# Performance work log

Measured on AMD Instinct MI355X. Metric: run time of the kernel, lower is better.

## Reference

```python
import jax, jax.numpy as jnp
import numpy as np

PLOGIT_INIT = 1.5

def setup_inputs() -> dict:
    key = jax.random.key(0)
    B, C, H, W = 32, 256, 64, 64
    x = jax.random.normal(key, (B, C, H, W), dtype=jnp.float32)
    plogit = jnp.full((C,), PLOGIT_INIT, dtype=jnp.float32)  # learned param (post channel-expansion)
    return {"input": x, "plogit": plogit}


def reference(input, plogit):
    B, C = input.shape[0], input.shape[1]
    x = input.reshape(B * C, -1)                       # [B*C, HW]  (to_cw)
    s = jnp.sort(x, axis=-1)                           # per-row full sort
    N = s.shape[1]
    p = jax.nn.sigmoid(plogit)                         # [C]
    # torch: p.view(1,-1).repeat(B,1).view(-1) -> channel-major tiling over batch
    p_full = jnp.tile(p, B)                            # [B*C]
    # torch indexes with int(N * p.data[0] -/+ 0.02): a single scalar column index
    p0 = jax.lax.stop_gradient(p[0])
    i_low = jnp.clip((N * (p0 - 0.02)).astype(jnp.int32), 0, N - 1)
    i_high = jnp.clip((N * (p0 + 0.02)).astype(jnp.int32), 0, N - 1)
    x_low = jax.lax.stop_gradient(jnp.take(s, i_low, axis=1))    # [B*C], detached
    x_high = jax.lax.stop_gradient(jnp.take(s, i_high, axis=1))  # [B*C], detached
    thr = x_low + (x_high - x_low) * p_full            # linear interp, grad flows via p
    thr = thr.reshape(B, C, 1, 1)                      # from_cw
    return jax.nn.relu(input - thr)
```

## Files before the change

kernel.cpp:

```cpp
#include <hip/hip_runtime.h>
#include <math.h>

#define NTHREADS 256
#define WPB      4
#define NELEM    4096
#define EPL      64
#define NREP1    4
#define HSTRIDE  260
#define WAVE_LDS (NREP1 * HSTRIDE)
#define LDSW     (WPB * WAVE_LDS)

typedef float v4f __attribute__((ext_vector_type(4)));

__device__ __forceinline__ unsigned f2ord(float f) {
    unsigned u = __float_as_uint(f);
    return u ^ ((unsigned)((int)u >> 31) | 0x80000000u);
}
__device__ __forceinline__ float ord2f(unsigned k) {
    return __uint_as_float(k ^ (~(unsigned)((int)k >> 31) | 0x80000000u));
}

__device__ __forceinline__ unsigned iscan_dpp(unsigned v) {
    v += (unsigned)__builtin_amdgcn_update_dpp(0, (int)v, 0x111, 0xF, 0xF, false);
    v += (unsigned)__builtin_amdgcn_update_dpp(0, (int)v, 0x112, 0xF, 0xF, false);
    v += (unsigned)__builtin_amdgcn_update_dpp(0, (int)v, 0x114, 0xF, 0xF, false);
    v += (unsigned)__builtin_amdgcn_update_dpp(0, (int)v, 0x118, 0xF, 0xF, false);
    v += (unsigned)__builtin_amdgcn_update_dpp(0, (int)v, 0x142, 0xA, 0xF, false);
    v += (unsigned)__builtin_amdgcn_update_dpp(0, (int)v, 0x143, 0xC, 0xF, false);
    return v;
}

struct Pick2 { unsigned a, b; };

template <int NR>
__device__ __forceinline__ Pick2 wave_pick2(const unsigned* region, int lane,
                                            unsigned rA, unsigned rB) {
    unsigned s0 = 0, s1 = 0, s2 = 0, s3 = 0;
    #pragma unroll
    for (int rep = 0; rep < NR; ++rep) {
        uint4 h = ((const uint4*)(region + rep * HSTRIDE))[lane];
        s0 += h.x; s1 += h.y; s2 += h.z; s3 += h.w;
    }
    unsigned tot = s0 + s1 + s2 + s3;
    unsigned inc = iscan_dpp(tot);
    unsigned ex  = inc - tot;
    unsigned base[4] = {ex, ex + s0, ex + s0 + s1, ex + s0 + s1 + s2};
    unsigned cnt[4]  = {s0, s1, s2, s3};
    unsigned resA = 0, resB = 0;
    bool fA = false, fB = false;
    #pragma unroll
    for (int j = 0; j < 4; ++j) {
        if (rA >= base[j] && rA < base[j] + cnt[j]) {
            resA = ((unsigned)(4 * lane + j) << 12) | (rA - base[j]); fA = true;
        }
        if (rB >= base[j] && rB < base[j] + cnt[j]) {
            resB = ((unsigned)(4 * lane + j) << 12) | (rB - base[j]); fB = true;
        }
    }
    unsigned long long mA = __ballot(fA);
    unsigned long long mB = __ballot(fB);
    Pick2 r;
    r.a = (unsigned)__builtin_amdgcn_readlane((int)resA, (int)(__ffsll((long long)mA) - 1));
    r.b = (unsigned)__builtin_amdgcn_readlane((int)resB, (int)(__ffsll((long long)mB) - 1));
    return r;
}

__global__ void __launch_bounds__(NTHREADS, 4)
xsrelu_kernel(const float* __restrict__ x, const float* __restrict__ plogit,
              float* __restrict__ out, int C, int nrows) {
    __shared__ __align__(16) unsigned hist[LDSW];

    const int tid  = threadIdx.x;
    const int wid  = tid >> 6;
    const int lane = tid & 63;
    const int row  = blockIdx.x * WPB + wid;
    if (row >= nrows) return;

    unsigned* wbase = hist + wid * WAVE_LDS;

    const float4* xr = (const float4*)(x + (size_t)row * NELEM);
    unsigned k[EPL];
    #pragma unroll
    for (int j = 0; j < EPL / 4; ++j) {
        float4 v = xr[j * 64 + lane];
        k[4 * j + 0] = f2ord(v.x);
        k[4 * j + 1] = f2ord(v.y);
        k[4 * j + 2] = f2ord(v.z);
        k[4 * j + 3] = f2ord(v.w);
    }

    float p0 = 1.0f / (1.0f + expf(-plogit[0]));
    float pc = 1.0f / (1.0f + expf(-plogit[row % C]));
    int kLow  = min(max((int)((float)NELEM * (p0 - 0.02f)), 0), NELEM - 1);
    int kHigh = min(max((int)((float)NELEM * (p0 + 0.02f)), 0), NELEM - 1);

    unsigned* my1 = wbase + (lane & (NREP1 - 1)) * HSTRIDE;
    const uint4 z4 = make_uint4(0u, 0u, 0u, 0u);
    #pragma unroll
    for (int r = 0; r < NREP1; ++r)
        ((uint4*)(wbase + r * HSTRIDE))[lane] = z4;
    #pragma unroll
    for (int j = 0; j < EPL; ++j)
        atomicAdd(&my1[k[j] >> 24], 1u);
    Pick2 p1 = wave_pick2<NREP1>(wbase, lane, (unsigned)kLow, (unsigned)kHigh);
    unsigned bA = p1.a >> 12, bB = p1.b >> 12;
    unsigned prefA = bA << 24, rA = p1.a & 0xFFFu;
    unsigned prefB = bB << 24, rB = p1.b & 0xFFFu;
    unsigned known = 0xFF000000u;
    bool diverged = (bA != bB);

    unsigned* myT = wbase;
    unsigned* myB = wbase + HSTRIDE;
    #pragma unroll 1
    for (int shift = 16; shift >= 0; shift -= 8) {
        if (!diverged) {
            ((uint4*)myT)[lane] = z4;
            #pragma unroll
            for (int j = 0; j < EPL; ++j) {
                unsigned kk = k[j];
                if ((kk & known) == prefA)
                    atomicAdd(&myT[(kk >> shift) & 0xFFu], 1u);
            }
            Pick2 p = wave_pick2<1>(myT, lane, rA, rB);
            unsigned cA = p.a >> 12, cB = p.b >> 12;
            prefA |= cA << shift;  rA = p.a & 0xFFFu;
            prefB |= cB << shift;  rB = p.b & 0xFFFu;
            diverged = (cA != cB);
        } else {
            ((uint4*)myT)[lane] = z4;
            ((uint4*)myB)[lane] = z4;
            #pragma unroll
            for (int j = 0; j < EPL; ++j) {
                unsigned kk = k[j];
                unsigned km = kk & known;
                bool isB = (km == prefB);
                if ((km == prefA) | isB)
                    atomicAdd((isB ? myB : myT) + ((kk >> shift) & 0xFFu), 1u);
            }
            unsigned pa = wave_pick2<1>(myT, lane, rA, rA).a;
            unsigned pb = wave_pick2<1>(myB, lane, rB, rB).a;
            prefA |= (pa >> 12) << shift;  rA = pa & 0xFFFu;
            prefB |= (pb >> 12) << shift;  rB = pb & 0xFFFu;
        }
        known |= 0xFFu << shift;
    }

    float xlow  = ord2f(prefA);
    float xhigh = ord2f(prefB);
    float thr = xlow + (xhigh - xlow) * pc;

    v4f* outr = (v4f*)(out + (size_t)row * NELEM);
    #pragma unroll
    for (int j = 0; j < EPL / 4; ++j) {
        v4f o;
        o.x = fmaxf(ord2f(k[4 * j + 0]) - thr, 0.0f);
        o.y = fmaxf(ord2f(k[4 * j + 1]) - thr, 0.0f);
        o.z = fmaxf(ord2f(k[4 * j + 2]) - thr, 0.0f);
        o.w = fmaxf(ord2f(k[4 * j + 3]) - thr, 0.0f);
        __builtin_nontemporal_store(o, outr + j * 64 + lane);
    }
}

extern "C" void kernel_launch(void* const* d_in, const int* in_sizes, int n_in,
                              void* d_out, int out_size, void* d_ws, size_t ws_size,
                              hipStream_t stream) {
    const float* x      = (const float*)d_in[0];
    const float* plogit = (const float*)d_in[1];
    float* out          = (float*)d_out;
    int C    = in_sizes[1];
    int rows = in_sizes[0] / NELEM;
    int grid = (rows + WPB - 1) / WPB;
    xsrelu_kernel<<<grid, NTHREADS, 0, stream>>>(x, plogit, out, C, rows);
}
```

Measured before the change: 237.6 us.

## Split into block-per-row threshold kernel and separate streaming ReLU kernel

Replaces the single fused kernel, in which each wave handled one row with 64 keys held in registers, by two kernels. The first assigns one 256-thread block per row, stores the ordered keys in LDS and builds block-shared radix histograms with __syncthreads between passes, then writes a per-row threshold to workspace. The second is a grid-stride elementwise kernel that rereads x and applies relu(x - thr). The aim is to cut register pressure and raise parallelism in the selection phase, at the cost of reading x from memory a second time, adding a kernel launch, and adding block-wide barriers.

```diff
diff --git a/kernel.cpp b/kernel.cpp
--- a/kernel.cpp
+++ b/kernel.cpp
@@ -1,14 +1,14 @@
 #include <hip/hip_runtime.h>
 #include <math.h>
 
-#define NTHREADS 256
-#define WPB      4
 #define NELEM    4096
-#define EPL      64
-#define NREP1    4
+#define A_THREADS 256
 #define HSTRIDE  260
-#define WAVE_LDS (NREP1 * HSTRIDE)
-#define LDSW     (WPB * WAVE_LDS)
+#define NHREP    8
+#define A_LDSW   (NELEM + NHREP * HSTRIDE)
+
+#define B_THREADS 256
+#define B_BLOCKS  2048
 
 typedef float v4f __attribute__((ext_vector_type(4)));
 
@@ -65,99 +65,110 @@
     return r;
 }
 
-__global__ void __launch_bounds__(NTHREADS, 4)
-xsrelu_kernel(const float* __restrict__ x, const float* __restrict__ plogit,
-              float* __restrict__ out, int C, int nrows) {
-    __shared__ __align__(16) unsigned hist[LDSW];
+__global__ void __launch_bounds__(A_THREADS, 4)
+thr_kernel(const float* __restrict__ x, const float* __restrict__ plogit,
+           float* __restrict__ thr_out, int C) {
+    __shared__ __align__(16) unsigned keys[NELEM];
+    __shared__ __align__(16) unsigned hist[NHREP * HSTRIDE];
 
     const int tid  = threadIdx.x;
     const int wid  = tid >> 6;
     const int lane = tid & 63;
-    const int row  = blockIdx.x * WPB + wid;
-    if (row >= nrows) return;
-
-    unsigned* wbase = hist + wid * WAVE_LDS;
+    const int row  = blockIdx.x;
 
     const float4* xr = (const float4*)(x + (size_t)row * NELEM);
-    unsigned k[EPL];
+    unsigned* myrep = hist + wid * HSTRIDE;
+    const uint4 z4 = make_uint4(0u, 0u, 0u, 0u);
+
+    ((uint4*)myrep)[lane] = z4;
     #pragma unroll
-    for (int j = 0; j < EPL / 4; ++j) {
-        float4 v = xr[j * 64 + lane];
-        k[4 * j + 0] = f2ord(v.x);
-        k[4 * j + 1] = f2ord(v.y);
-        k[4 * j + 2] = f2ord(v.z);
-        k[4 * j + 3] = f2ord(v.w);
+    for (int j = 0; j < 4; ++j) {
+        int idx = wid * 256 + j * 64 + lane;
+        float4 v = xr[idx];
+        unsigned k0 = f2ord(v.x), k1 = f2ord(v.y), k2 = f2ord(v.z), k3 = f2ord(v.w);
+        ((uint4*)keys)[idx] = make_uint4(k0, k1, k2, k3);
+        atomicAdd(&myrep[k0 >> 24], 1u);
+        atomicAdd(&myrep[k1 >> 24], 1u);
+        atomicAdd(&myrep[k2 >> 24], 1u);
+        atomicAdd(&myrep[k3 >> 24], 1u);
     }
 
     float p0 = 1.0f / (1.0f + expf(-plogit[0]));
     float pc = 1.0f / (1.0f + expf(-plogit[row % C]));
-    int kLow  = min(max((int)((float)NELEM * (p0 - 0.02f)), 0), NELEM - 1);
-    int kHigh = min(max((int)((float)NELEM * (p0 + 0.02f)), 0), NELEM - 1);
+    unsigned kLow  = (unsigned)min(max((int)((float)NELEM * (p0 - 0.02f)), 0), NELEM - 1);
+    unsigned kHigh = (unsigned)min(max((int)((float)NELEM * (p0 + 0.02f)), 0), NELEM - 1);
 
-    unsigned* my1 = wbase + (lane & (NREP1 - 1)) * HSTRIDE;
-    const uint4 z4 = make_uint4(0u, 0u, 0u, 0u);
-    #pragma unroll
-    for (int r = 0; r < NREP1; ++r)
-        ((uint4*)(wbase + r * HSTRIDE))[lane] = z4;
-    #pragma unroll
-    for (int j = 0; j < EPL; ++j)
-        atomicAdd(&my1[k[j] >> 24], 1u);
-    Pick2 p1 = wave_pick2<NREP1>(wbase, lane, (unsigned)kLow, (unsigned)kHigh);
+    __syncthreads();
+    Pick2 p1 = wave_pick2<4>(hist, lane, kLow, kHigh);
     unsigned bA = p1.a >> 12, bB = p1.b >> 12;
     unsigned prefA = bA << 24, rA = p1.a & 0xFFFu;
     unsigned prefB = bB << 24, rB = p1.b & 0xFFFu;
     unsigned known = 0xFF000000u;
     bool diverged = (bA != bB);
 
-    unsigned* myT = wbase;
-    unsigned* myB = wbase + HSTRIDE;
     #pragma unroll 1
     for (int shift = 16; shift >= 0; shift -= 8) {
+        __syncthreads();
+        ((uint4*)myrep)[lane] = z4;
+        if (diverged) ((uint4*)(myrep + 4 * HSTRIDE))[lane] = z4;
+        #pragma unroll
+        for (int j = 0; j < 4; ++j) {
+            uint4 kk4 = ((const uint4*)keys)[wid * 256 + j * 64 + lane];
+            unsigned ks[4] = {kk4.x, kk4.y, kk4.z, kk4.w};
+            #pragma unroll
+            for (int e = 0; e < 4; ++e) {
+                unsigned kk = ks[e];
+                unsigned km = kk & known;
+                if (!diverged) {
+                    if (km == prefA)
+                        atomicAdd(&myrep[(kk >> shift) & 0xFFu], 1u);
+                } else {
+                    bool isB = (km == prefB);
+                    if ((km == prefA) | isB)
+                        atomicAdd(myrep + (isB ? 4 * HSTRIDE : 0)
+                                        + ((kk >> shift) & 0xFFu), 1u);
+                }
+            }
+        }
+        __syncthreads();
         if (!diverged) {
-            ((uint4*)myT)[lane] = z4;
-            #pragma unroll
-            for (int j = 0; j < EPL; ++j) {
-                unsigned kk = k[j];
-                if ((kk & known) == prefA)
-                    atomicAdd(&myT[(kk >> shift) & 0xFFu], 1u);
-            }
-            Pick2 p = wave_pick2<1>(myT, lane, rA, rB);
+            Pick2 p = wave_pick2<4>(hist, lane, rA, rB);
             unsigned cA = p.a >> 12, cB = p.b >> 12;
             prefA |= cA << shift;  rA = p.a & 0xFFFu;
             prefB |= cB << shift;  rB = p.b & 0xFFFu;
             diverged = (cA != cB);
         } else {
-            ((uint4*)myT)[lane] = z4;
-            ((uint4*)myB)[lane] = z4;
-            #pragma unroll
-            for (int j = 0; j < EPL; ++j) {
-                unsigned kk = k[j];
-                unsigned km = kk & known;
-                bool isB = (km == prefB);
-                if ((km == prefA) | isB)
-                    atomicAdd((isB ? myB : myT) + ((kk >> shift) & 0xFFu), 1u);
-            }
-            unsigned pa = wave_pick2<1>(myT, lane, rA, rA).a;
-            unsigned pb = wave_pick2<1>(myB, lane, rB, rB).a;
+            unsigned pa = wave_pick2<4>(hist, lane, rA, rA).a;
+            unsigned pb = wave_pick2<4>(hist + 4 * HSTRIDE, lane, rB, rB).a;
             prefA |= (pa >> 12) << shift;  rA = pa & 0xFFFu;
             prefB |= (pb >> 12) << shift;  rB = pb & 0xFFFu;
         }
         known |= 0xFFu << shift;
     }
 
-    float xlow  = ord2f(prefA);
-    float xhigh = ord2f(prefB);
-    float thr = xlow + (xhigh - xlow) * pc;
+    if (tid == 0) {
+        float xlow  = ord2f(prefA);
+        float xhigh = ord2f(prefB);
+        thr_out[row] = xlow + (xhigh - xlow) * pc;
+    }
+}
 
-    v4f* outr = (v4f*)(out + (size_t)row * NELEM);
-    #pragma unroll
-    for (int j = 0; j < EPL / 4; ++j) {
+__global__ void __launch_bounds__(B_THREADS)
+relu_kernel(const float* __restrict__ x, const float* __restrict__ thr,
+            float* __restrict__ out, long total4) {
+    long i = (long)blockIdx.x * B_THREADS + threadIdx.x;
+    const long stride = (long)gridDim.x * B_THREADS;
+    const float4* xv = (const float4*)x;
+    v4f* ov = (v4f*)out;
+    for (; i < total4; i += stride) {
+        float4 v = xv[i];
+        float t = thr[i >> 10];
         v4f o;
-        o.x = fmaxf(ord2f(k[4 * j + 0]) - thr, 0.0f);
-        o.y = fmaxf(ord2f(k[4 * j + 1]) - thr, 0.0f);
-        o.z = fmaxf(ord2f(k[4 * j + 2]) - thr, 0.0f);
-        o.w = fmaxf(ord2f(k[4 * j + 3]) - thr, 0.0f);
-        __builtin_nontemporal_store(o, outr + j * 64 + lane);
+        o.x = fmaxf(v.x - t, 0.0f);
+        o.y = fmaxf(v.y - t, 0.0f);
+        o.z = fmaxf(v.z - t, 0.0f);
+        o.w = fmaxf(v.w - t, 0.0f);
+        __builtin_nontemporal_store(o, ov + i);
     }
 }
 
@@ -167,8 +178,10 @@
     const float* x      = (const float*)d_in[0];
     const float* plogit = (const float*)d_in[1];
     float* out          = (float*)d_out;
+    float* thr          = (float*)d_ws;
     int C    = in_sizes[1];
     int rows = in_sizes[0] / NELEM;
-    int grid = (rows + WPB - 1) / WPB;
-    xsrelu_kernel<<<grid, NTHREADS, 0, stream>>>(x, plogit, out, C, rows);
+    thr_kernel<<<rows, A_THREADS, 0, stream>>>(x, plogit, thr, C);
+    long total4 = (long)rows * (NELEM / 4);
+    relu_kernel<<<B_BLOCKS, B_THREADS, 0, stream>>>(x, thr, out, total4);
 }
```

Measured after the change: 281.4 us. 1.18x slower.

## Replace multi-pass radix histogram select with compaction plus bitwise ballot search

Applied to the files above, without the earlier changes.

After the first 8-bit histogram pass, the keys falling in buckets between the low and high target buckets are compacted into a small per-wave LDS buffer. The remaining 24 bits are then resolved by a bitwise binary search that counts with ballot and popcount, which removes the later histogram passes and their LDS atomics. The histogram layout also changes to bin-strided per-lane reads, with four separate DPP scans. If the candidate set overflows the buffer, the search falls back to ballots over all 64 register keys per bit, which costs far more per pass.

```diff
diff --git a/kernel.cpp b/kernel.cpp
--- a/kernel.cpp
+++ b/kernel.cpp
@@ -5,9 +5,12 @@
 #define WPB      4
 #define NELEM    4096
 #define EPL      64
-#define NREP1    4
-#define HSTRIDE  260
-#define WAVE_LDS (NREP1 * HSTRIDE)
+#define NREP     4
+#define RSTRIDE  260
+#define CBUF_OFF (NREP * RSTRIDE)
+#define CAP      768
+#define MAXS     (CAP / 64)
+#define WAVE_LDS (CBUF_OFF + CAP)
 #define LDSW     (WPB * WAVE_LDS)
 
 typedef float v4f __attribute__((ext_vector_type(4)));
@@ -30,45 +33,51 @@
     return v;
 }
 
-struct Pick2 { unsigned a, b; };
-
-template <int NR>
-__device__ __forceinline__ Pick2 wave_pick2(const unsigned* region, int lane,
-                                            unsigned rA, unsigned rB) {
+struct PickB { unsigned bktA, bktB, baseA; };
+
+__device__ __forceinline__ PickB pick_dual(const unsigned* hist, int lane,
+                                           unsigned rA, unsigned rB) {
     unsigned s0 = 0, s1 = 0, s2 = 0, s3 = 0;
     #pragma unroll
-    for (int rep = 0; rep < NR; ++rep) {
-        uint4 h = ((const uint4*)(region + rep * HSTRIDE))[lane];
-        s0 += h.x; s1 += h.y; s2 += h.z; s3 += h.w;
-    }
-    unsigned tot = s0 + s1 + s2 + s3;
-    unsigned inc = iscan_dpp(tot);
-    unsigned ex  = inc - tot;
-    unsigned base[4] = {ex, ex + s0, ex + s0 + s1, ex + s0 + s1 + s2};
-    unsigned cnt[4]  = {s0, s1, s2, s3};
+    for (int rep = 0; rep < NREP; ++rep) {
+        const unsigned* h = hist + rep * RSTRIDE;
+        s0 += h[lane];
+        s1 += h[64 + lane];
+        s2 += h[128 + lane];
+        s3 += h[192 + lane];
+    }
+    unsigned c0 = iscan_dpp(s0), c1 = iscan_dpp(s1);
+    unsigned c2 = iscan_dpp(s2), c3 = iscan_dpp(s3);
+    unsigned T0 = (unsigned)__builtin_amdgcn_readlane((int)c0, 63);
+    unsigned T1 = (unsigned)__builtin_amdgcn_readlane((int)c1, 63);
+    unsigned T2 = (unsigned)__builtin_amdgcn_readlane((int)c2, 63);
+    unsigned e0 = c0 - s0;
+    unsigned e1 = T0 + c1 - s1;
+    unsigned e2 = T0 + T1 + c2 - s2;
+    unsigned e3 = T0 + T1 + T2 + c3 - s3;
+    unsigned ex[4]  = {e0, e1, e2, e3};
+    unsigned cnt[4] = {s0, s1, s2, s3};
     unsigned resA = 0, resB = 0;
     bool fA = false, fB = false;
     #pragma unroll
     for (int j = 0; j < 4; ++j) {
-        if (rA >= base[j] && rA < base[j] + cnt[j]) {
-            resA = ((unsigned)(4 * lane + j) << 12) | (rA - base[j]); fA = true;
-        }
-        if (rB >= base[j] && rB < base[j] + cnt[j]) {
-            resB = ((unsigned)(4 * lane + j) << 12) | (rB - base[j]); fB = true;
-        }
+        unsigned bin = (unsigned)(j * 64 + lane);
+        if (rA >= ex[j] && rA < ex[j] + cnt[j]) { resA = (bin << 13) | ex[j]; fA = true; }
+        if (rB >= ex[j] && rB < ex[j] + cnt[j]) { resB = (bin << 13) | ex[j]; fB = true; }
     }
     unsigned long long mA = __ballot(fA);
     unsigned long long mB = __ballot(fB);
-    Pick2 r;
-    r.a = (unsigned)__builtin_amdgcn_readlane((int)resA, (int)(__ffsll((long long)mA) - 1));
-    r.b = (unsigned)__builtin_amdgcn_readlane((int)resB, (int)(__ffsll((long long)mB) - 1));
+    unsigned a = (unsigned)__builtin_amdgcn_readlane((int)resA, (int)(__ffsll((long long)mA) - 1));
+    unsigned b = (unsigned)__builtin_amdgcn_readlane((int)resB, (int)(__ffsll((long long)mB) - 1));
+    PickB r;
+    r.bktA = a >> 13; r.baseA = a & 0x1FFFu; r.bktB = b >> 13;
     return r;
 }
 
 __global__ void __launch_bounds__(NTHREADS, 4)
 xsrelu_kernel(const float* __restrict__ x, const float* __restrict__ plogit,
               float* __restrict__ out, int C, int nrows) {
-    __shared__ __align__(16) unsigned hist[LDSW];
+    __shared__ __align__(16) unsigned lds[LDSW];
 
     const int tid  = threadIdx.x;
     const int wid  = tid >> 6;
@@ -76,7 +85,8 @@
     const int row  = blockIdx.x * WPB + wid;
     if (row >= nrows) return;
 
-    unsigned* wbase = hist + wid * WAVE_LDS;
+    unsigned* wbase = lds + wid * WAVE_LDS;
+    unsigned* cbuf  = wbase + CBUF_OFF;
 
     const float4* xr = (const float4*)(x + (size_t)row * NELEM);
     unsigned k[EPL];
@@ -91,62 +101,83 @@
 
     float p0 = 1.0f / (1.0f + expf(-plogit[0]));
     float pc = 1.0f / (1.0f + expf(-plogit[row % C]));
-    int kLow  = min(max((int)((float)NELEM * (p0 - 0.02f)), 0), NELEM - 1);
-    int kHigh = min(max((int)((float)NELEM * (p0 + 0.02f)), 0), NELEM - 1);
-
-    unsigned* my1 = wbase + (lane & (NREP1 - 1)) * HSTRIDE;
-    const uint4 z4 = make_uint4(0u, 0u, 0u, 0u);
-    #pragma unroll
-    for (int r = 0; r < NREP1; ++r)
-        ((uint4*)(wbase + r * HSTRIDE))[lane] = z4;
+    unsigned kLow  = (unsigned)min(max((int)((float)NELEM * (p0 - 0.02f)), 0), NELEM - 1);
+    unsigned kHigh = (unsigned)min(max((int)((float)NELEM * (p0 + 0.02f)), 0), NELEM - 1);
+
+    #pragma unroll
+    for (int r = 0; r < NREP; ++r) {
+        unsigned* h = wbase + r * RSTRIDE;
+        h[lane] = 0u; h[64 + lane] = 0u; h[128 + lane] = 0u; h[192 + lane] = 0u;
+    }
+    unsigned* my = wbase + (lane & (NREP - 1)) * RSTRIDE;
     #pragma unroll
     for (int j = 0; j < EPL; ++j)
-        atomicAdd(&my1[k[j] >> 24], 1u);
-    Pick2 p1 = wave_pick2<NREP1>(wbase, lane, (unsigned)kLow, (unsigned)kHigh);
-    unsigned bA = p1.a >> 12, bB = p1.b >> 12;
-    unsigned prefA = bA << 24, rA = p1.a & 0xFFFu;
-    unsigned prefB = bB << 24, rB = p1.b & 0xFFFu;
-    unsigned known = 0xFF000000u;
-    bool diverged = (bA != bB);
-
-    unsigned* myT = wbase;
-    unsigned* myB = wbase + HSTRIDE;
-    #pragma unroll 1
-    for (int shift = 16; shift >= 0; shift -= 8) {
-        if (!diverged) {
-            ((uint4*)myT)[lane] = z4;
+        atomicAdd(&my[k[j] >> 24], 1u);
+
+    PickB p = pick_dual(wbase, lane, kLow, kHigh);
+    unsigned bktA = p.bktA, bktB = p.bktB, baseA = p.baseA;
+    unsigned span = bktB - bktA;
+
+    unsigned mlo = 0u, mhi = 0u, mycnt = 0u;
+    #pragma unroll
+    for (int j = 0; j < EPL; ++j) {
+        bool m = ((k[j] >> 24) - bktA) <= span;
+        mycnt += m ? 1u : 0u;
+        if (j < 32) mlo |= m ? (1u << j) : 0u;
+        else        mhi |= m ? (1u << (j - 32)) : 0u;
+    }
+    unsigned inc  = iscan_dpp(mycnt);
+    unsigned scnt = (unsigned)__builtin_amdgcn_readlane((int)inc, 63);
+
+    unsigned keyA, keyB;
+    if (scnt <= CAP) {
+        unsigned wpos = inc - mycnt;
+        #pragma unroll
+        for (int j = 0; j < EPL; ++j) {
+            bool m = (j < 32) ? ((mlo >> j) & 1u) : ((mhi >> (j - 32)) & 1u);
+            if (m) { cbuf[wpos] = k[j]; ++wpos; }
+        }
+        unsigned S[MAXS];
+        #pragma unroll
+        for (int j = 0; j < MAXS; ++j) {
+            unsigned idx = (unsigned)(j * 64 + lane);
+            unsigned w = cbuf[idx];
+            S[j] = (idx < scnt) ? w : 0xFFFFFFFFu;
+        }
+        unsigned pA = bktA << 24, pB = bktB << 24;
+        unsigned lrA = kLow - baseA, lrB = kHigh - baseA;
+        #pragma unroll 1
+        for (int b = 23; b >= 0; --b) {
+            unsigned cA = pA | (1u << b), cB = pB | (1u << b);
+            unsigned nA = 0, nB = 0;
+            #pragma unroll
+            for (int j = 0; j < MAXS; ++j) {
+                nA += (unsigned)__popcll(__ballot(S[j] < cA));
+                nB += (unsigned)__popcll(__ballot(S[j] < cB));
+            }
+            if (nA <= lrA) pA = cA;
+            if (nB <= lrB) pB = cB;
+        }
+        keyA = pA; keyB = pB;
+    } else {
+        unsigned pA = bktA << 24, pB = bktB << 24;
+        #pragma unroll 1
+        for (int b = 23; b >= 0; --b) {
+            unsigned cA = pA | (1u << b), cB = pB | (1u << b);
+            unsigned nA = 0, nB = 0;
             #pragma unroll
             for (int j = 0; j < EPL; ++j) {
-                unsigned kk = k[j];
-                if ((kk & known) == prefA)
-                    atomicAdd(&myT[(kk >> shift) & 0xFFu], 1u);
+                nA += (unsigned)__popcll(__ballot(k[j] < cA));
+                nB += (unsigned)__popcll(__ballot(k[j] < cB));
             }
-            Pick2 p = wave_pick2<1>(myT, lane, rA, rB);
-            unsigned cA = p.a >> 12, cB = p.b >> 12;
-            prefA |= cA << shift;  rA = p.a & 0xFFFu;
-            prefB |= cB << shift;  rB = p.b & 0xFFFu;
-            diverged = (cA != cB);
-        } else {
-            ((uint4*)myT)[lane] = z4;
-            ((uint4*)myB)[lane] = z4;
-            #pragma unroll
-            for (int j = 0; j < EPL; ++j) {
-                unsigned kk = k[j];
-                unsigned km = kk & known;
-                bool isB = (km == prefB);
-                if ((km == prefA) | isB)
-                    atomicAdd((isB ? myB : myT) + ((kk >> shift) & 0xFFu), 1u);
-            }
-            unsigned pa = wave_pick2<1>(myT, lane, rA, rA).a;
-            unsigned pb = wave_pick2<1>(myB, lane, rB, rB).a;
-            prefA |= (pa >> 12) << shift;  rA = pa & 0xFFFu;
-            prefB |= (pb >> 12) << shift;  rB = pb & 0xFFFu;
-        }
-        known |= 0xFFu << shift;
-    }
-
-    float xlow  = ord2f(prefA);
-    float xhigh = ord2f(prefB);
+            if (nA <= kLow)  pA = cA;
+            if (nB <= kHigh) pB = cB;
+        }
+        keyA = pA; keyB = pB;
+    }
+
+    float xlow  = ord2f(keyA);
+    float xhigh = ord2f(keyB);
     float thr = xlow + (xhigh - xlow) * pc;
 
     v4f* outr = (v4f*)(out + (size_t)row * NELEM);
```

After: 298.8 us. +25.8%, slower.

## Process rows per block cooperatively with double-buffered async LDS row prefetch

Applied to the files above, without the earlier changes.

Moves from one wave per row to all four waves of a block sharing each row. Each wave loads a quarter of the row and bumps a shared 4-replica histogram, and each block walks 8 rows in sequence. The next row is prefetched into LDS with global_load_lds, double-buffered and tracked by explicit vmcnt waits, so the load overlaps the radix-select on the current row. This cuts registers per thread from 64 keys to 16 and hides load latency. The cost is block barriers on every radix pass, a grid eight times smaller, 32KB of LDS per block and a fragile hand-written wait-count scheme.

```diff
diff --git a/kernel.cpp b/kernel.cpp
--- a/kernel.cpp
+++ b/kernel.cpp
@@ -2,15 +2,27 @@
 #include <math.h>
 
 #define NTHREADS 256
-#define WPB      4
+#define ROWS_PB  8
 #define NELEM    4096
-#define EPL      64
-#define NREP1    4
+#define QUART    1024
+#define KPL      16
+#define NREP     4
 #define HSTRIDE  260
-#define WAVE_LDS (NREP1 * HSTRIDE)
-#define LDSW     (WPB * WAVE_LDS)
-
-typedef float v4f __attribute__((ext_vector_type(4)));
+#define HISTW    (NREP * HSTRIDE)
+
+__device__ __forceinline__ void syncw() {
+    asm volatile("s_waitcnt lgkmcnt(0)" ::: "memory");
+    __builtin_amdgcn_s_barrier();
+}
+__device__ __forceinline__ void wait_vm(int n) {
+    switch (n) {
+        case 0:  asm volatile("s_waitcnt vmcnt(0)"  ::: "memory"); break;
+        case 4:  asm volatile("s_waitcnt vmcnt(4)"  ::: "memory"); break;
+        case 16: asm volatile("s_waitcnt vmcnt(16)" ::: "memory"); break;
+        default: asm volatile("s_waitcnt vmcnt(20)" ::: "memory"); break;
+    }
+    __builtin_amdgcn_sched_barrier(0);
+}
 
 __device__ __forceinline__ unsigned f2ord(float f) {
     unsigned u = __float_as_uint(f);
@@ -30,134 +42,148 @@
     return v;
 }
 
-struct Pick2 { unsigned a, b; };
-
-template <int NR>
-__device__ __forceinline__ Pick2 wave_pick2(const unsigned* region, int lane,
-                                            unsigned rA, unsigned rB) {
+struct PickR { unsigned binA, baseA, binB, baseB; };
+
+__device__ __forceinline__ PickR pick_dual(const unsigned* h, int lane,
+                                           unsigned rA, unsigned rB) {
     unsigned s0 = 0, s1 = 0, s2 = 0, s3 = 0;
     #pragma unroll
-    for (int rep = 0; rep < NR; ++rep) {
-        uint4 h = ((const uint4*)(region + rep * HSTRIDE))[lane];
-        s0 += h.x; s1 += h.y; s2 += h.z; s3 += h.w;
-    }
-    unsigned tot = s0 + s1 + s2 + s3;
-    unsigned inc = iscan_dpp(tot);
-    unsigned ex  = inc - tot;
-    unsigned base[4] = {ex, ex + s0, ex + s0 + s1, ex + s0 + s1 + s2};
-    unsigned cnt[4]  = {s0, s1, s2, s3};
+    for (int rep = 0; rep < NREP; ++rep) {
+        const unsigned* r = h + rep * HSTRIDE;
+        s0 += r[lane]; s1 += r[64 + lane]; s2 += r[128 + lane]; s3 += r[192 + lane];
+    }
+    unsigned c0 = iscan_dpp(s0), c1 = iscan_dpp(s1);
+    unsigned c2 = iscan_dpp(s2), c3 = iscan_dpp(s3);
+    unsigned T0 = (unsigned)__builtin_amdgcn_readlane((int)c0, 63);
+    unsigned T1 = (unsigned)__builtin_amdgcn_readlane((int)c1, 63);
+    unsigned T2 = (unsigned)__builtin_amdgcn_readlane((int)c2, 63);
+    unsigned ex[4] = {c0 - s0, T0 + c1 - s1, T0 + T1 + c2 - s2, T0 + T1 + T2 + c3 - s3};
+    unsigned cn[4] = {s0, s1, s2, s3};
     unsigned resA = 0, resB = 0;
     bool fA = false, fB = false;
     #pragma unroll
     for (int j = 0; j < 4; ++j) {
-        if (rA >= base[j] && rA < base[j] + cnt[j]) {
-            resA = ((unsigned)(4 * lane + j) << 12) | (rA - base[j]); fA = true;
-        }
-        if (rB >= base[j] && rB < base[j] + cnt[j]) {
-            resB = ((unsigned)(4 * lane + j) << 12) | (rB - base[j]); fB = true;
-        }
+        unsigned bin = (unsigned)(j * 64 + lane);
+        if (rA >= ex[j] && rA < ex[j] + cn[j]) { resA = (bin << 13) | ex[j]; fA = true; }
+        if (rB >= ex[j] && rB < ex[j] + cn[j]) { resB = (bin << 13) | ex[j]; fB = true; }
     }
     unsigned long long mA = __ballot(fA);
     unsigned long long mB = __ballot(fB);
-    Pick2 r;
-    r.a = (unsigned)__builtin_amdgcn_readlane((int)resA, (int)(__ffsll((long long)mA) - 1));
-    r.b = (unsigned)__builtin_amdgcn_readlane((int)resB, (int)(__ffsll((long long)mB) - 1));
+    unsigned a = (unsigned)__builtin_amdgcn_readlane((int)resA, (int)(__ffsll((long long)mA) - 1));
+    unsigned b = (unsigned)__builtin_amdgcn_readlane((int)resB, (int)(__ffsll((long long)mB) - 1));
+    PickR r;
+    r.binA = a >> 13; r.baseA = a & 0x1FFFu;
+    r.binB = b >> 13; r.baseB = b & 0x1FFFu;
     return r;
+}
+
+__device__ __forceinline__ void dma4(const float* g, float* l, int lane) {
+    #pragma unroll
+    for (int i = 0; i < 4; ++i) {
+        __builtin_amdgcn_global_load_lds(
+            (const __attribute__((address_space(1))) void*)(g + i * 256 + lane * 4),
+            (__attribute__((address_space(3))) void*)(l + i * 256),
+            16, 0, 0);
+    }
 }
 
 __global__ void __launch_bounds__(NTHREADS, 4)
 xsrelu_kernel(const float* __restrict__ x, const float* __restrict__ plogit,
               float* __restrict__ out, int C, int nrows) {
-    __shared__ __align__(16) unsigned hist[LDSW];
+    __shared__ __align__(16) float    buf[2][NELEM];
+    __shared__ __align__(16) unsigned hist[HISTW];
 
     const int tid  = threadIdx.x;
     const int wid  = tid >> 6;
     const int lane = tid & 63;
-    const int row  = blockIdx.x * WPB + wid;
-    if (row >= nrows) return;
-
-    unsigned* wbase = hist + wid * WAVE_LDS;
-
-    const float4* xr = (const float4*)(x + (size_t)row * NELEM);
-    unsigned k[EPL];
-    #pragma unroll
-    for (int j = 0; j < EPL / 4; ++j) {
-        float4 v = xr[j * 64 + lane];
-        k[4 * j + 0] = f2ord(v.x);
-        k[4 * j + 1] = f2ord(v.y);
-        k[4 * j + 2] = f2ord(v.z);
-        k[4 * j + 3] = f2ord(v.w);
-    }
+    const int row0 = blockIdx.x * ROWS_PB;
+    if (row0 >= nrows) return;
+    const int rp = min(ROWS_PB, nrows - row0);
 
     float p0 = 1.0f / (1.0f + expf(-plogit[0]));
-    float pc = 1.0f / (1.0f + expf(-plogit[row % C]));
-    int kLow  = min(max((int)((float)NELEM * (p0 - 0.02f)), 0), NELEM - 1);
-    int kHigh = min(max((int)((float)NELEM * (p0 + 0.02f)), 0), NELEM - 1);
-
-    unsigned* my1 = wbase + (lane & (NREP1 - 1)) * HSTRIDE;
-    const uint4 z4 = make_uint4(0u, 0u, 0u, 0u);
-    #pragma unroll
-    for (int r = 0; r < NREP1; ++r)
-        ((uint4*)(wbase + r * HSTRIDE))[lane] = z4;
-    #pragma unroll
-    for (int j = 0; j < EPL; ++j)
-        atomicAdd(&my1[k[j] >> 24], 1u);
-    Pick2 p1 = wave_pick2<NREP1>(wbase, lane, (unsigned)kLow, (unsigned)kHigh);
-    unsigned bA = p1.a >> 12, bB = p1.b >> 12;
-    unsigned prefA = bA << 24, rA = p1.a & 0xFFFu;
-    unsigned prefB = bB << 24, rB = p1.b & 0xFFFu;
-    unsigned known = 0xFF000000u;
-    bool diverged = (bA != bB);
-
-    unsigned* myT = wbase;
-    unsigned* myB = wbase + HSTRIDE;
+    unsigned kLow  = (unsigned)min(max((int)((float)NELEM * (p0 - 0.02f)), 0), NELEM - 1);
+    unsigned kHigh = (unsigned)min(max((int)((float)NELEM * (p0 + 0.02f)), 0), NELEM - 1);
+
+    unsigned* rep = hist + wid * HSTRIDE;
+
+    dma4(x + (size_t)row0 * NELEM + wid * QUART, buf[0] + wid * QUART, lane);
+
     #pragma unroll 1
-    for (int shift = 16; shift >= 0; shift -= 8) {
-        if (!diverged) {
-            ((uint4*)myT)[lane] = z4;
+    for (int n = 0; n < rp; ++n) {
+        if (n + 1 < rp)
+            dma4(x + (size_t)(row0 + n + 1) * NELEM + wid * QUART,
+                 buf[(n + 1) & 1] + wid * QUART, lane);
+
+        if (n == 0)            wait_vm(rp > 1 ? 4 : 0);
+        else if (n + 1 < rp)   wait_vm(20);
+        else                   wait_vm(16);
+
+        const float* bc = buf[n & 1] + wid * QUART;
+        unsigned k[KPL];
+        #pragma unroll
+        for (int j = 0; j < KPL; ++j)
+            k[j] = f2ord(bc[j * 64 + lane]);
+
+        rep[lane] = 0u; rep[64 + lane] = 0u; rep[128 + lane] = 0u; rep[192 + lane] = 0u;
+        #pragma unroll
+        for (int j = 0; j < KPL; ++j)
+            atomicAdd(&rep[k[j] >> 24], 1u);
+        syncw();
+        PickR p = pick_dual(hist, lane, kLow, kHigh);
+        syncw();
+        unsigned prefA = p.binA << 24, lrA = kLow  - p.baseA;
+        unsigned prefB = p.binB << 24, lrB = kHigh - p.baseB;
+        int divshift = (p.binA != p.binB) ? 24 : -1;
+        unsigned maskA = 0xFF000000u;
+
+        #pragma unroll 1
+        for (int shift = 16; shift >= 0; shift -= 8) {
+            rep[lane] = 0u; rep[64 + lane] = 0u; rep[128 + lane] = 0u; rep[192 + lane] = 0u;
             #pragma unroll
-            for (int j = 0; j < EPL; ++j) {
-                unsigned kk = k[j];
-                if ((kk & known) == prefA)
-                    atomicAdd(&myT[(kk >> shift) & 0xFFu], 1u);
+            for (int j = 0; j < KPL; ++j)
+                if ((k[j] & maskA) == prefA)
+                    atomicAdd(&rep[(k[j] >> shift) & 0xFFu], 1u);
+            syncw();
+            if (divshift < 0) {
+                PickR q = pick_dual(hist, lane, lrA, lrB);
+                syncw();
+                prefA |= q.binA << shift; lrA -= q.baseA;
+                prefB |= q.binB << shift; lrB -= q.baseB;
+                if (q.binA != q.binB) divshift = shift;
+            } else {
+                PickR q = pick_dual(hist, lane, lrA, lrA);
+                syncw();
+                prefA |= q.binA << shift; lrA -= q.baseA;
             }
-            Pick2 p = wave_pick2<1>(myT, lane, rA, rB);
-            unsigned cA = p.a >> 12, cB = p.b >> 12;
-            prefA |= cA << shift;  rA = p.a & 0xFFFu;
-            prefB |= cB << shift;  rB = p.b & 0xFFFu;
-            diverged = (cA != cB);
-        } else {
-            ((uint4*)myT)[lane] = z4;
-            ((uint4*)myB)[lane] = z4;
-            #pragma unroll
-            for (int j = 0; j < EPL; ++j) {
-                unsigned kk = k[j];
-                unsigned km = kk & known;
-                bool isB = (km == prefB);
-                if ((km == prefA) | isB)
-                    atomicAdd((isB ? myB : myT) + ((kk >> shift) & 0xFFu), 1u);
+            maskA |= 0xFFu << shift;
+        }
+
+        if (divshift > 0) {
+            unsigned maskB = 0xFFFFFFFFu << divshift;
+            #pragma unroll 1
+            for (int shift = divshift - 8; shift >= 0; shift -= 8) {
+                rep[lane] = 0u; rep[64 + lane] = 0u; rep[128 + lane] = 0u; rep[192 + lane] = 0u;
+                #pragma unroll
+                for (int j = 0; j < KPL; ++j)
+                    if ((k[j] & maskB) == prefB)
+                        atomicAdd(&rep[(k[j] >> shift) & 0xFFu], 1u);
+                syncw();
+                PickR q = pick_dual(hist, lane, lrB, lrB);
+                syncw();
+                prefB |= q.binA << shift; lrB -= q.baseA;
+                maskB |= 0xFFu << shift;
             }
-            unsigned pa = wave_pick2<1>(myT, lane, rA, rA).a;
-            unsigned pb = wave_pick2<1>(myB, lane, rB, rB).a;
-            prefA |= (pa >> 12) << shift;  rA = pa & 0xFFFu;
-            prefB |= (pb >> 12) << shift;  rB = pb & 0xFFFu;
         }
-        known |= 0xFFu << shift;
-    }
-
-    float xlow  = ord2f(prefA);
-    float xhigh = ord2f(prefB);
-    float thr = xlow + (xhigh - xlow) * pc;
-
-    v4f* outr = (v4f*)(out + (size_t)row * NELEM);
-    #pragma unroll
-    for (int j = 0; j < EPL / 4; ++j) {
-        v4f o;
-        o.x = fmaxf(ord2f(k[4 * j + 0]) - thr, 0.0f);
-        o.y = fmaxf(ord2f(k[4 * j + 1]) - thr, 0.0f);
-        o.z = fmaxf(ord2f(k[4 * j + 2]) - thr, 0.0f);
-        o.w = fmaxf(ord2f(k[4 * j + 3]) - thr, 0.0f);
-        __builtin_nontemporal_store(o, outr + j * 64 + lane);
+
+        int row = row0 + n;
+        float pc = 1.0f / (1.0f + expf(-plogit[row % C]));
+        float xlow = ord2f(prefA), xhigh = ord2f(prefB);
+        float thr = xlow + (xhigh - xlow) * pc;
+        float* orow = out + (size_t)row * NELEM + wid * QUART;
+        #pragma unroll
+        for (int j = 0; j < KPL; ++j)
+            __builtin_nontemporal_store(fmaxf(ord2f(k[j]) - thr, 0.0f),
+                                        &orow[j * 64 + lane]);
     }
 }
 
@@ -169,6 +195,6 @@
     float* out          = (float*)d_out;
     int C    = in_sizes[1];
     int rows = in_sizes[0] / NELEM;
-    int grid = (rows + WPB - 1) / WPB;
+    int grid = (rows + ROWS_PB - 1) / ROWS_PB;
     xsrelu_kernel<<<grid, NTHREADS, 0, stream>>>(x, plogit, out, C, rows);
 }
```

New measurement: 282.6 us. 1.19x slower.
